# Kernel optimization log

Hardware: AMD Instinct MI355X
Metric: run time of the kernel (lower is better)

The kernel has to match this reference:

```python
import jax, jax.numpy as jnp
import numpy as np

B, C, H, W = 64, 256, 14, 14
K = 9
HID = 256   # EdgeAgg hidden_channels = in_channels
OUT = 512   # out_channels = 2*in_channels (required by final reshape)


def _knn(q, kset, k):
    # ViG dense_knn_matrix: squared-distance knn, top-k of -dist (self-loop may be included)
    qs = jnp.sum(q * q, -1)
    ks = jnp.sum(kset * kset, -1)
    dist = qs[:, :, None] - 2.0 * jnp.einsum('bnc,bmc->bnm', q, kset) + ks[:, None, :]
    _, idx = jax.lax.top_k(-dist, k)   # (B,N,k) neighbor indices into kset
    return idx


def _edgeconv_add(feat, nbr, validf, w, b):
    # PyG EdgeConv(nn=Linear, aggr='add') with per-node valid-edge mask:
    #   out[i] = sum_{j in valid nbrs(i)} cat(x_i, x_j - x_i) @ w + b
    # nn is linear, so aggregate neighbor diffs BEFORE the matmul (same math, less traffic).
    Cf = feat.shape[-1]
    wa, wb = w[:Cf], w[Cf:]
    deg = jnp.sum(validf, -1, keepdims=True)                   # (B,N,1)
    xj = feat[jnp.arange(feat.shape[0])[:, None, None], nbr]   # (B,N,k,C) gather
    sum_xj = jnp.einsum('bnkc,bnk->bnc', xj, validf)
    return deg * (feat @ wa + b) + (sum_xj - deg * feat) @ wb


def _forward(x, fc1_w, fc1_b, fc2_w, fc2_b, fce_w, fce_b, inout_w, inout_b,
             attn_w, attn_b, upd_w, upd_b, kp_w, kp_b, enc_w, enc_b,
             mu_w, mu_b, dec_w, dec_b, T):
    k = dec_w.shape[-1]
    b_, c_, h_, w_ = x.shape
    n = h_ * w_
    xs = x.reshape(b_, c_, n)                       # (B,C,N)
    x_sp = jnp.transpose(xs, (0, 2, 1))             # (B,N,C) true spatial node feats for knn
    x_sp_d = jax.lax.stop_gradient(x_sp)            # original detaches before knn
    x_nbr = _knn(x_sp_d, x_sp_d, k)
    # temporal roll across the T frames of each clip
    y_sp = jnp.roll(x_sp.reshape(b_ // T, T, n, c_), -1, axis=1).reshape(b_, n, c_)
    y_nbr = _knn(x_sp_d, jax.lax.stop_gradient(y_sp), k)
    # faithful to original: x.view(B*N, C) reinterprets the contiguous (B,C,N) buffer
    x_feat = xs.reshape(b_, n, c_)
    y_feat = jnp.transpose(y_sp, (0, 2, 1)).reshape(b_, n, c_)
    # VAE-like K predictor (deterministic z = mu); argmax -> per-node degree in [0,k)
    hk = x_feat.reshape(b_ * n, c_) @ kp_w + kp_b
    hk = jax.nn.relu(hk @ enc_w + enc_b)
    mu = hk @ mu_w + mu_b
    logits = mu @ dec_w + dec_b                     # (B*N, k)
    k_int = jnp.argmax(logits, axis=1)
    # generate_mask: keep the first k_int[i] of node i's k edges
    validf = (jnp.arange(k)[None, :] < k_int[:, None]).astype(x.dtype).reshape(b_, n, k)

    def edge_agg(feat, nbr):
        h1 = jax.nn.relu(_edgeconv_add(feat, nbr, validf, fc1_w, fc1_b))
        h2 = _edgeconv_add(h1, nbr, validf, fc2_w, fc2_b)
        return (h2 @ fce_w + fce_b).reshape(b_ * n, -1)

    x_agg = edge_agg(x_feat, x_nbr)
    y_agg = edge_agg(y_feat, y_nbr)
    scores = (jnp.concatenate([x_agg, y_agg], -1) @ attn_w + attn_b)[:, 0]
    wgt = jax.nn.softmax(scores, axis=0)[:, None]   # softmax over ALL B*N nodes (as in source)
    fused = wgt * x_agg + (1.0 - wgt) * y_agg
    xin = x_feat.reshape(b_ * n, c_) @ inout_w + inout_b
    upd = jax.nn.relu(jnp.concatenate([xin, fused], -1) @ upd_w + upd_b)   # (B*N, 2C)
    return jnp.transpose(upd.reshape(b_, n, 2 * c_), (0, 2, 1)).reshape(b_, 2 * c_, h_, w_)


def setup_inputs():
    key = jax.random.key(0)
    ks = iter(jax.random.split(key, 32))

    def lin(i, o):
        return jax.random.normal(next(ks), (i, o), jnp.float32) / np.sqrt(i)

    def bias(o):
        return jax.random.normal(next(ks), (o,), jnp.float32) * 0.01

    return {
        'x': jax.random.normal(next(ks), (B, C, H, W), jnp.float32),
        'fc1_w': lin(2 * C, HID), 'fc1_b': bias(HID),
        'fc2_w': lin(2 * HID, HID), 'fc2_b': bias(HID),
        'fce_w': lin(HID, OUT), 'fce_b': bias(OUT),
        'inout_w': lin(C, OUT), 'inout_b': bias(OUT),
        'attn_w': lin(2 * OUT, 1), 'attn_b': bias(1),
        'upd_w': lin(2 * OUT, OUT), 'upd_b': bias(OUT),
        'kp_w': lin(C, 500), 'kp_b': bias(500),
        'enc_w': lin(500, 64), 'enc_b': bias(64),
        'mu_w': lin(64, 32), 'mu_b': bias(32),
        'dec_w': lin(32, K), 'dec_b': bias(K),
        'T': 16,
    }


def reference(x, fc1_w, fc1_b, fc2_w, fc2_b, fce_w, fce_b, inout_w, inout_b,
              attn_w, attn_b, upd_w, upd_b, kp_w, kp_b, enc_w, enc_b,
              mu_w, mu_b, dec_w, dec_b, T):
    return _forward(x, fc1_w, fc1_b, fc2_w, fc2_b, fce_w, fce_b, inout_w, inout_b,
                    attn_w, attn_b, upd_w, upd_b, kp_w, kp_b, enc_w, enc_b,
                    mu_w, mu_b, dec_w, dec_b, T)
```

## Files before the change

kernel.cpp:

```cpp
#include <hip/hip_runtime.h>
#include <cstddef>
#include <cstdint>

constexpr int BATCH = 64;
constexpr int CH    = 256;
constexpr int NPT   = 196;
constexpr int ROWS  = BATCH * NPT;
constexpr int BSTRIDE = CH * NPT;
constexpr int KNB   = 8;
constexpr int DSTR  = 208;

typedef __bf16 bf16x8 __attribute__((ext_vector_type(8)));
typedef __bf16 bf16x4 __attribute__((ext_vector_type(4)));
typedef _Float16 f16x8 __attribute__((ext_vector_type(8)));
typedef float  f32x4  __attribute__((ext_vector_type(4)));
typedef unsigned long long u64;

__device__ __forceinline__ int src_batch(int b) {
    return (b & ~15) | ((b + 1) & 15);
}

__device__ __forceinline__ void gload_lds16(const void* g, void* l) {
    __builtin_amdgcn_global_load_lds(
        (const __attribute__((address_space(1))) void*)g,
        (__attribute__((address_space(3))) void*)l, 16, 0, 0);
}

__device__ __forceinline__ int xcd_swz(int lin, int nwg) {
    int q = nwg >> 3;
    return (lin & 7) * q + (lin >> 3);
}

__global__ __launch_bounds__(256) void front_kernel(const float* __restrict__ x,
        _Float16* __restrict__ XH, _Float16* __restrict__ XL,
        __bf16* __restrict__ XB, float* __restrict__ qs,
        const float* __restrict__ fc1_w, const float* __restrict__ fc2_w,
        const float* __restrict__ fce_w, const float* __restrict__ upd_w,
        const float* __restrict__ kp_w, const float* __restrict__ kp_b,
        const float* __restrict__ enc_w, const float* __restrict__ enc_b,
        const float* __restrict__ mu_w, const float* __restrict__ mu_b,
        const float* __restrict__ dec_w, const float* __restrict__ dec_b,
        const float* __restrict__ inout_w, const float* __restrict__ inout_b,
        const float* __restrict__ upd_b,
        __bf16* __restrict__ W1catT, __bf16* __restrict__ W2catT,
        __bf16* __restrict__ fcet, __bf16* __restrict__ updC,
        float* __restrict__ KW1, float* __restrict__ kb1,
        float* __restrict__ KW2, float* __restrict__ kb2,
        float* __restrict__ bcomp, int* __restrict__ smcnt) {
    __shared__ __attribute__((aligned(16))) char smem[16896];
    float (*tile)[65] = (float(*)[65])smem;
    int bid = blockIdx.x;
    int t = threadIdx.x;
    if (bid < 1024) {
        int m0 = (bid & 3) * 64, c0 = ((bid >> 2) & 3) * 64, b = bid >> 4;
        const float* xb = x + (size_t)b * BSTRIDE;
        #pragma unroll
        for (int s = 0; s < 16; ++s) {
            int idx = s * 256 + t;
            int cc = idx >> 6, mm = idx & 63;
            int m = m0 + mm;
            float v = (m < NPT) ? xb[(size_t)(c0 + cc) * NPT + m] : 0.f;
            tile[cc][mm] = v;
            if (m < NPT)
                XB[(size_t)b * BSTRIDE + (size_t)(c0 + cc) * NPT + m] = (__bf16)v;
        }
        __syncthreads();
        #pragma unroll
        for (int s = 0; s < 16; ++s) {
            int idx = s * 256 + t;
            int mm = idx >> 6, cc = idx & 63;
            float v = tile[cc][mm];
            _Float16 h = (_Float16)v;
            size_t off = ((size_t)b * 256 + (m0 + mm)) * 256 + c0 + cc;
            XH[off] = h;
            XL[off] = (_Float16)(v - (float)h);
        }
    } else if (bid < 1088) {
        int b = bid - 1024;
        int m = t;
        if (m >= NPT) return;
        const float* xb = x + (size_t)b * BSTRIDE;
        float acc = 0.f;
        for (int c = 0; c < CH; ++c) {
            float v = xb[c * NPT + m];
            acc = fmaf(v, v, acc);
        }
        qs[b * NPT + m] = acc;
    } else {
        int pbid = bid - 1088;
        if (pbid == 0 && t == 0) smcnt[0] = 0;
        if (pbid < 64) {
            const float* W = (pbid < 32) ? fc1_w : fc2_w;
            __bf16* WT = (pbid < 32) ? W1catT : W2catT;
            int local = pbid & 31;
            int n0 = (local >> 2) * 64, k0 = (local & 3) * 64;
            #pragma unroll
            for (int s = 0; s < 16; ++s) {
                int idx = s * 256 + t;
                int kk = idx >> 6, nn = idx & 63;
                float v;
                if (n0 < 256)
                    v = W[(size_t)(k0 + kk) * 256 + n0 + nn] -
                        W[(size_t)(k0 + kk + 256) * 256 + n0 + nn];
                else
                    v = W[(size_t)(k0 + kk + 256) * 256 + (n0 - 256) + nn];
                tile[kk][nn] = v;
            }
            __syncthreads();
            #pragma unroll
            for (int s = 0; s < 16; ++s) {
                int idx = s * 256 + t;
                int nn = idx >> 6, kk = idx & 63;
                WT[(size_t)(n0 + nn) * 256 + k0 + kk] = (__bf16)tile[kk][nn];
            }
        } else if (pbid < 96) {
            int local = pbid - 64;
            int n0 = (local >> 2) * 64, k0 = (local & 3) * 64;
            #pragma unroll
            for (int s = 0; s < 16; ++s) {
                int idx = s * 256 + t;
                int kk = idx >> 6, nn = idx & 63;
                tile[kk][nn] = fce_w[(size_t)(k0 + kk) * 512 + n0 + nn];
            }
            __syncthreads();
            #pragma unroll
            for (int s = 0; s < 16; ++s) {
                int idx = s * 256 + t;
                int nn = idx >> 6, kk = idx & 63;
                fcet[(size_t)(n0 + nn) * 256 + k0 + kk] = (__bf16)tile[kk][nn];
            }
        } else if (pbid < 160) {
            int local = pbid - 96;
            int k0 = (local >> 3) * 64, n0 = (local & 7) * 64;
            #pragma unroll
            for (int s = 0; s < 16; ++s) {
                int idx = s * 256 + t;
                int kk = idx >> 6, nn = idx & 63;
                tile[kk][nn] = upd_w[(size_t)(512 + k0 + kk) * 512 + n0 + nn];
            }
            __syncthreads();
            #pragma unroll
            for (int s = 0; s < 16; ++s) {
                int idx = s * 256 + t;
                int nn = idx >> 6, kk = idx & 63;
                updC[(size_t)(n0 + nn) * 768 + 256 + k0 + kk] = (__bf16)tile[kk][nn];
            }
        } else if (pbid < 224) {
            int i = (pbid - 160) * 4 + (t >> 6);
            int j = t & 63;
            double acc = 0.0;
            for (int k = 0; k < 500; ++k)
                acc += (double)kp_w[(size_t)i * 500 + k] * (double)enc_w[(size_t)k * 64 + j];
            KW1[i * 64 + j] = (float)acc;
        } else if (pbid == 224) {
            int j = t;
            if (j < 64) {
                double acc = (double)enc_b[j];
                for (int k = 0; k < 500; ++k)
                    acc += (double)kp_b[k] * (double)enc_w[(size_t)k * 64 + j];
                kb1[j] = (float)acc;
            }
        } else if (pbid < 228) {
            int e = (pbid - 225) * 256 + t;
            if (e < 576) {
                int i = e / 9, j = e - (e / 9) * 9;
                double acc = 0.0;
                for (int k = 0; k < 32; ++k)
                    acc += (double)mu_w[(size_t)i * 32 + k] * (double)dec_w[(size_t)k * 9 + j];
                KW2[e] = (float)acc;
            } else if (e < 585) {
                int j = e - 576;
                double acc = (double)dec_b[j];
                for (int k = 0; k < 32; ++k)
                    acc += (double)mu_b[k] * (double)dec_w[(size_t)k * 9 + j];
                kb2[j] = (float)acc;
            }
        } else if (pbid < 740) {
            int e = (pbid - 228) * 256 + t;
            int k = e >> 9, n = e & 511;
            double acc = 0.0;
            for (int j = 0; j < 512; ++j)
                acc += (double)inout_w[(size_t)k * 512 + j] * (double)upd_w[(size_t)j * 512 + n];
            updC[(size_t)n * 768 + k] = (__bf16)(float)acc;
        } else {
            int n = (pbid - 740) * 256 + t;
            double acc = (double)upd_b[n];
            for (int j = 0; j < 512; ++j)
                acc += (double)inout_b[j] * (double)upd_w[(size_t)j * 512 + n];
            bcomp[n] = (float)acc;
        }
    }
}

__global__ __launch_bounds__(256) void gram_kint(const _Float16* __restrict__ XH,
        const _Float16* __restrict__ XL, const float* __restrict__ qs,
        float* __restrict__ Dw, const float* __restrict__ x,
        const float* __restrict__ W1, const float* __restrict__ b1,
        const float* __restrict__ W2, const float* __restrict__ b2,
        int* __restrict__ kint, float* __restrict__ degf) {
    __shared__ __attribute__((aligned(16))) char smem[21056];
    int bid = blockIdx.x;
    int t = threadIdx.x;
    if (bid < 2048) {
        _Float16* Ah = (_Float16*)smem;
        _Float16* Al = Ah + 2048;
        _Float16* Bh = Al + 2048;
        _Float16* Bl = Bh + 2048;
        int nid = xcd_swz(bid, 2048);
        int job = nid >> 4;
        int tile = nid & 15;
        int by = tile >> 2, bx = tile & 3;
        int r0 = by * 64, c0 = bx * 64;
        int qb = (job < 64) ? job : job - 64;
        int kb = (job < 64) ? qb : src_batch(qb);
        int w = t >> 6, l = t & 63;
        int lr = l & 15, lg = l >> 4;
        int wr = (w >> 1) * 32, wc = (w & 1) * 32;
        const _Float16* qh = XH + (size_t)qb * 65536;
        const _Float16* ql = XL + (size_t)qb * 65536;
        const _Float16* kh = XH + (size_t)kb * 65536;
        const _Float16* kl = XL + (size_t)kb * 65536;
        f32x4 acc[2][2] = {};
        for (int k0 = 0; k0 < 256; k0 += 32) {
            {
                int row = w * 16 + (l >> 2);
                int cb = (l & 3) * 8;
                size_t goA = (size_t)(r0 + row) * 256 + k0 + cb;
                size_t goB = (size_t)(c0 + row) * 256 + k0 + cb;
                gload_lds16(qh + goA, Ah + w * 512);
                gload_lds16(ql + goA, Al + w * 512);
                gload_lds16(kh + goB, Bh + w * 512);
                gload_lds16(kl + goB, Bl + w * 512);
            }
            asm volatile("s_waitcnt vmcnt(0)" ::: "memory");
            __syncthreads();
            f16x8 ah[2], alv[2], bh[2], blv[2];
            #pragma unroll
            for (int mi = 0; mi < 2; ++mi) {
                ah[mi]  = *(const f16x8*)(Ah + (wr + mi * 16 + lr) * 32 + lg * 8);
                alv[mi] = *(const f16x8*)(Al + (wr + mi * 16 + lr) * 32 + lg * 8);
            }
            #pragma unroll
            for (int ni = 0; ni < 2; ++ni) {
                bh[ni]  = *(const f16x8*)(Bh + (wc + ni * 16 + lr) * 32 + lg * 8);
                blv[ni] = *(const f16x8*)(Bl + (wc + ni * 16 + lr) * 32 + lg * 8);
            }
            #pragma unroll
            for (int mi = 0; mi < 2; ++mi)
                #pragma unroll
                for (int ni = 0; ni < 2; ++ni) {
                    acc[mi][ni] = __builtin_amdgcn_mfma_f32_16x16x32_f16(
                        ah[mi], bh[ni], acc[mi][ni], 0, 0, 0);
                    acc[mi][ni] = __builtin_amdgcn_mfma_f32_16x16x32_f16(
                        ah[mi], blv[ni], acc[mi][ni], 0, 0, 0);
                    acc[mi][ni] = __builtin_amdgcn_mfma_f32_16x16x32_f16(
                        alv[mi], bh[ni], acc[mi][ni], 0, 0, 0);
                }
            __syncthreads();
        }
        const float* qsq = qs + qb * NPT;
        const float* qsk = qs + kb * NPT;
        float ksv[2];
        #pragma unroll
        for (int ni = 0; ni < 2; ++ni) {
            int col = c0 + wc + ni * 16 + lr;
            ksv[ni] = (col < NPT) ? qsk[col] : 0.f;
        }
        #pragma unroll
        for (int mi = 0; mi < 2; ++mi) {
            #pragma unroll
            for (int r = 0; r < 4; ++r) {
                if (r0 + wr + mi * 16 + r >= NPT) continue;
                int grow = r0 + wr + mi * 16 + lg * 4 + r;
                if (grow >= NPT) continue;
                float qq = qsq[grow];
                size_t rbase = ((size_t)job * NPT + grow) * DSTR;
                #pragma unroll
                for (int ni = 0; ni < 2; ++ni) {
                    int col = c0 + wc + ni * 16 + lr;
                    if (col < NPT)
                        Dw[rbase + col] = qq - 2.f * acc[mi][ni][r] + ksv[ni];
                }
            }
        }
    } else {
        float (*xr)[256] = (float(*)[256])smem;
        float (*ebuf)[64] = (float(*)[64])(smem + 16384);
        float (*lg2)[9]  = (float(*)[9])(smem + 20480);
        int r0 = (bid - 2048) * 16;
        const float4* xg = (const float4*)(x + (size_t)r0 * 256);
        float4* xs = (float4*)&xr[0][0];
        #pragma unroll
        for (int s = 0; s < 4; ++s) xs[s * 256 + t] = xg[s * 256 + t];
        __syncthreads();
        int w = t >> 6, l = t & 63;
        {
            float bb = b1[l];
            float a0 = bb, a1 = bb, a2 = bb, a3 = bb;
            const float* x0 = xr[w * 4 + 0];
            const float* x1 = xr[w * 4 + 1];
            const float* x2 = xr[w * 4 + 2];
            const float* x3 = xr[w * 4 + 3];
            for (int c = 0; c < 256; ++c) {
                float wv = W1[c * 64 + l];
                a0 = fmaf(x0[c], wv, a0);
                a1 = fmaf(x1[c], wv, a1);
                a2 = fmaf(x2[c], wv, a2);
                a3 = fmaf(x3[c], wv, a3);
            }
            ebuf[w * 4 + 0][l] = fmaxf(a0, 0.f);
            ebuf[w * 4 + 1][l] = fmaxf(a1, 0.f);
            ebuf[w * 4 + 2][l] = fmaxf(a2, 0.f);
            ebuf[w * 4 + 3][l] = fmaxf(a3, 0.f);
        }
        __syncthreads();
        int rr = t >> 4, cc = t & 15;
        if (cc < 9) {
            float acc = b2[cc];
            for (int j = 0; j < 64; ++j)
                acc = fmaf(ebuf[rr][j], W2[j * 9 + cc], acc);
            lg2[rr][cc] = acc;
        }
        __syncthreads();
        if (cc == 0) {
            float best = lg2[rr][0];
            int bi = 0;
            #pragma unroll
            for (int j = 1; j < 9; ++j)
                if (lg2[rr][j] > best) { best = lg2[rr][j]; bi = j; }
            kint[r0 + rr] = bi;
            degf[r0 + rr] = (float)bi;
        }
    }
}

__global__ __launch_bounds__(256) void topk_kernel(const float* __restrict__ Dw,
                                                   int* __restrict__ nbr) {
    __shared__ u64 lists[64][4][8];
    int t = threadIdx.x;
    int lrow = t >> 2, q = t & 3;
    int rowid = blockIdx.x * 64 + lrow;
    const float* rp = Dw + (size_t)rowid * DSTR + q * 52;
    u64 kreg[8];
    #pragma unroll
    for (int p = 0; p < 8; ++p) kreg[p] = ~0ull;
    for (int s4 = 0; s4 < 13; ++s4) {
        f32x4 dv = *(const f32x4*)(rp + s4 * 4);
        #pragma unroll
        for (int e = 0; e < 4; ++e) {
            int col = q * 52 + s4 * 4 + e;
            unsigned u = __float_as_uint(dv[e]);
            u = (u & 0x80000000u) ? ~u : (u | 0x80000000u);
            u64 key = (col < NPT) ? (((u64)u << 32) | (unsigned)col) : ~0ull;
            if (key < kreg[7]) {
                #pragma unroll
                for (int p = 0; p < 8; ++p) {
                    u64 mn = (key < kreg[p]) ? key : kreg[p];
                    u64 mx = (key < kreg[p]) ? kreg[p] : key;
                    kreg[p] = mn; key = mx;
                }
            }
        }
    }
    #pragma unroll
    for (int p = 0; p < 8; ++p) lists[lrow][q][p] = kreg[p];
    __syncthreads();
    if (q == 0) {
        const u64* c = &lists[lrow][0][0];
        int p0 = 0, p1 = 0, p2 = 0, p3 = 0;
        #pragma unroll
        for (int it = 0; it < 8; ++it) {
            u64 v0 = c[p0], v1 = c[8 + p1], v2 = c[16 + p2], v3 = c[24 + p3];
            u64 best = v0; int bj = 0;
            if (v1 < best) { best = v1; bj = 1; }
            if (v2 < best) { best = v2; bj = 2; }
            if (v3 < best) { best = v3; bj = 3; }
            if (bj == 0) p0 = (p0 < 7) ? p0 + 1 : 7;
            else if (bj == 1) p1 = (p1 < 7) ? p1 + 1 : 7;
            else if (bj == 2) p2 = (p2 < 7) ? p2 + 1 : 7;
            else p3 = (p3 < 7) ? p3 + 1 : 7;
            nbr[(size_t)rowid * KNB + it] = (int)(best & 0xffffffffu);
        }
    }
}

template<int STAGE, int RELU>
__global__ __launch_bounds__(256) void combine_kernel(const __bf16* __restrict__ P,
        const int* __restrict__ nbr, const int* __restrict__ kint_,
        const float* __restrict__ degf, const float* __restrict__ bias,
        __bf16* __restrict__ H) {
    int g = threadIdx.x >> 6, lane = threadIdx.x & 63;
    int nid = xcd_swz(blockIdx.x, 2 * ROWS / 4);
    int r = nid * 4 + g;
    int branch = (r >= ROWS);
    int rr = r - branch * ROWS;
    int b = rr / NPT, i = rr - b * NPT;
    size_t srow, mbase;
    if constexpr (STAGE == 1) {
        int fb = branch ? src_batch(b) : b;
        srow = (size_t)fb * NPT + i;
        mbase = (size_t)fb * NPT;
    } else {
        srow = (size_t)r;
        mbase = (size_t)branch * ROWS + (size_t)b * NPT;
    }
    const int* nb = nbr + (size_t)branch * ((size_t)ROWS * KNB) + (size_t)rr * KNB;
    bf16x4 sv = *(const bf16x4*)(P + srow * 512 + lane * 4);
    float4 bv = *(const float4*)(bias + lane * 4);
    float s0 = 0.f, s1 = 0.f, s2 = 0.f, s3 = 0.f;
    int kk = kint_[rr];
    for (int tt = 0; tt < kk; ++tt) {
        int m = nb[tt];
        bf16x4 v = *(const bf16x4*)(P + (mbase + m) * 512 + 256 + lane * 4);
        s0 += (float)v[0]; s1 += (float)v[1]; s2 += (float)v[2]; s3 += (float)v[3];
    }
    float dg = degf[rr];
    float o0 = fmaf(dg, (float)sv[0] + bv.x, s0);
    float o1 = fmaf(dg, (float)sv[1] + bv.y, s1);
    float o2 = fmaf(dg, (float)sv[2] + bv.z, s2);
    float o3 = fmaf(dg, (float)sv[3] + bv.w, s3);
    if constexpr (RELU) {
        o0 = fmaxf(o0, 0.f); o1 = fmaxf(o1, 0.f);
        o2 = fmaxf(o2, 0.f); o3 = fmaxf(o3, 0.f);
    }
    bf16x4 ov;
    ov[0] = (__bf16)o0; ov[1] = (__bf16)o1; ov[2] = (__bf16)o2; ov[3] = (__bf16)o3;
    *(bf16x4*)(H + (size_t)r * 256 + lane * 4) = ov;
}

template<int FLAGS, int CONCAT>
__global__ __launch_bounds__(256) void mfma_gemm(
    const __bf16* __restrict__ A0, const __bf16* __restrict__ A1,
    const __bf16* __restrict__ WT, const float* __restrict__ bias,
    float* __restrict__ Cf, __bf16* __restrict__ Cb, int K, int N,
    const float* __restrict__ aw, float* __restrict__ scp,
    const float* __restrict__ wgt) {
    constexpr int SMEMB = (FLAGS & 8) ? (128 * 129 * 4) : (2 * 128 * 64 * 2);
    __shared__ __attribute__((aligned(16))) char smem[SMEMB];
    __bf16* As = (__bf16*)smem;
    __bf16* Bs = As + 128 * 64;
    int lin = blockIdx.x + 4 * blockIdx.y;
    int nid = xcd_swz(lin, 4 * gridDim.y);
    int bx = nid & 3, by = nid >> 2;
    int t = threadIdx.x, w = t >> 6, l = t & 63;
    int r0 = by * 128, c0 = bx * 128;
    int lr = l & 15, lg = l >> 4;
    int wr = (w >> 1) * 64, wc = (w & 1) * 64;
    f32x4 acc[4][4] = {};
    for (int k0 = 0; k0 < K; k0 += 64) {
        #pragma unroll
        for (int i = 0; i < 4; ++i) {
            int row = (w * 4 + i) * 8 + (l >> 3);
            int c8 = l & 7;
            if constexpr (CONCAT == 2) {
                if (k0 < 256) {
                    gload_lds16(A0 + (size_t)(r0 + row) * 256 + k0 + c8 * 8,
                                As + (w * 4 + i) * 512);
                } else {
                    int kk2 = k0 - 256 + c8 * 8;
                    size_t gr = (size_t)(r0 + row);
                    bf16x8 xa = *(const bf16x8*)(A1 + gr * 512 + kk2);
                    bf16x8 ya = *(const bf16x8*)(A1 + ((size_t)ROWS + gr) * 512 + kk2);
                    float wv = wgt[gr];
                    bf16x8 mx;
                    #pragma unroll
                    for (int j = 0; j < 8; ++j)
                        mx[j] = (__bf16)(wv * (float)xa[j] + (1.f - wv) * (float)ya[j]);
                    *(bf16x8*)(As + (w * 4 + i) * 512 + l * 8) = mx;
                }
            } else {
                gload_lds16(A0 + (size_t)(r0 + row) * K + k0 + c8 * 8,
                            As + (w * 4 + i) * 512);
            }
            gload_lds16(WT + (size_t)(c0 + row) * K + k0 + c8 * 8,
                        Bs + (w * 4 + i) * 512);
        }
        asm volatile("s_waitcnt vmcnt(0)" ::: "memory");
        __syncthreads();
        #pragma unroll
        for (int ks = 0; ks < 2; ++ks) {
            bf16x8 af[4], bfr[4];
            #pragma unroll
            for (int mi = 0; mi < 4; ++mi)
                af[mi] = *(const bf16x8*)(As + (wr + mi * 16 + lr) * 64 + ks * 32 + lg * 8);
            #pragma unroll
            for (int ni = 0; ni < 4; ++ni)
                bfr[ni] = *(const bf16x8*)(Bs + (wc + ni * 16 + lr) * 64 + ks * 32 + lg * 8);
            #pragma unroll
            for (int mi = 0; mi < 4; ++mi)
                #pragma unroll
                for (int ni = 0; ni < 4; ++ni)
                    acc[mi][ni] = __builtin_amdgcn_mfma_f32_16x16x32_bf16(
                        af[mi], bfr[ni], acc[mi][ni], 0, 0, 0);
        }
        __syncthreads();
    }
    if constexpr ((FLAGS & 8) != 0) {
        float* tile = (float*)smem;
        #pragma unroll
        for (int mi = 0; mi < 4; ++mi)
            #pragma unroll
            for (int r = 0; r < 4; ++r) {
                int rrow = wr + mi * 16 + lg * 4 + r;
                #pragma unroll
                for (int ni = 0; ni < 4; ++ni) {
                    int ccol = wc + ni * 16 + lr;
                    float v = acc[mi][ni][r];
                    if (bias) v += bias[c0 + ccol];
                    if constexpr ((FLAGS & 1) != 0) v = fmaxf(v, 0.f);
                    tile[rrow * 129 + ccol] = v;
                }
            }
        __syncthreads();
        int cc = t >> 6, rr2 = t & 63;
        #pragma unroll
        for (int cs = 0; cs < 128; cs += 4) {
            #pragma unroll
            for (int h = 0; h < 2; ++h) {
                int row = r0 + rr2 + h * 64;
                int bb = row / NPT, ii = row - bb * NPT;
                Cf[((size_t)bb * 512 + (c0 + cc + cs)) * NPT + ii] =
                    tile[(rr2 + h * 64) * 129 + cc + cs];
            }
        }
    } else if constexpr ((FLAGS & 16) != 0) {
        int half = (r0 >= ROWS) ? 1 : 0;
        float ps[4][4] = {};
        #pragma unroll
        for (int mi = 0; mi < 4; ++mi)
            #pragma unroll
            for (int r = 0; r < 4; ++r) {
                int row = r0 + wr + mi * 16 + lg * 4 + r;
                #pragma unroll
                for (int ni = 0; ni < 4; ++ni) {
                    int col = c0 + wc + ni * 16 + lr;
                    float v = acc[mi][ni][r] + bias[col];
                    Cb[(size_t)row * N + col] = (__bf16)v;
                    ps[mi][r] = fmaf(v, aw[half * 512 + col], ps[mi][r]);
                }
            }
        #pragma unroll
        for (int m = 1; m <= 8; m <<= 1)
            #pragma unroll
            for (int mi = 0; mi < 4; ++mi)
                #pragma unroll
                for (int r = 0; r < 4; ++r)
                    ps[mi][r] += __shfl_xor(ps[mi][r], m, 64);
        if (lr == 0) {
            int slot = half * 8 + bx * 2 + (w & 1);
            #pragma unroll
            for (int mi = 0; mi < 4; ++mi)
                #pragma unroll
                for (int r = 0; r < 4; ++r) {
                    int sr = r0 - half * ROWS + wr + mi * 16 + lg * 4 + r;
                    scp[(size_t)slot * ROWS + sr] = ps[mi][r];
                }
        }
    } else {
        #pragma unroll
        for (int mi = 0; mi < 4; ++mi) {
            #pragma unroll
            for (int r = 0; r < 4; ++r) {
                int row = r0 + wr + mi * 16 + lg * 4 + r;
                #pragma unroll
                for (int ni = 0; ni < 4; ++ni) {
                    int col = c0 + wc + ni * 16 + lr;
                    float v = acc[mi][ni][r];
                    if (bias) v += bias[col];
                    if constexpr ((FLAGS & 1) != 0) v = fmaxf(v, 0.f);
                    if constexpr ((FLAGS & 4) != 0)
                        Cb[(size_t)row * N + col] = (__bf16)v;
                    else
                        Cf[(size_t)row * N + col] = v;
                }
            }
        }
    }
}

__global__ __launch_bounds__(256) void softmax_all(const float* __restrict__ scp,
        const float* __restrict__ ab, float* __restrict__ scores,
        float* __restrict__ mpart, float* __restrict__ spart,
        int* __restrict__ cnt, float* __restrict__ wgt) {
    __shared__ float red[256];
    __shared__ float MS[2];
    __shared__ bool islast;
    int t = threadIdx.x;
    int sr = blockIdx.x * 256 + t;
    float s = ab[0];
    #pragma unroll
    for (int i = 0; i < 16; ++i) s += scp[(size_t)i * ROWS + sr];
    scores[sr] = s;
    red[t] = s; __syncthreads();
    for (int off = 128; off; off >>= 1) {
        if (t < off) red[t] = fmaxf(red[t], red[t + off]);
        __syncthreads();
    }
    float mb = red[0]; __syncthreads();
    red[t] = expf(s - mb); __syncthreads();
    for (int off = 128; off; off >>= 1) {
        if (t < off) red[t] += red[t + off];
        __syncthreads();
    }
    if (t == 0) {
        mpart[blockIdx.x] = mb;
        spart[blockIdx.x] = red[0];
        __threadfence();
        int old = atomicAdd(cnt, 1);
        islast = (old == 48);
    }
    __syncthreads();
    if (!islast) return;
    __threadfence();
    if (t == 0) {
        float M = mpart[0];
        for (int i = 1; i < 49; ++i) M = fmaxf(M, mpart[i]);
        float S = 0.f;
        for (int i = 0; i < 49; ++i) S += spart[i] * expf(mpart[i] - M);
        MS[0] = M; MS[1] = S;
        cnt[0] = 0;
    }
    __syncthreads();
    float M = MS[0], denom = MS[1];
    for (int i = t; i < ROWS; i += 256)
        wgt[i] = expf(scores[i] - M) / denom;
}

extern "C" void kernel_launch(void* const* d_in, const int* in_sizes, int n_in,
                              void* d_out, int out_size, void* d_ws, size_t ws_size,
                              hipStream_t stream) {
    (void)in_sizes; (void)n_in; (void)out_size; (void)ws_size;
    const float* x       = (const float*)d_in[0];
    const float* fc1_w   = (const float*)d_in[1];
    const float* fc1_b   = (const float*)d_in[2];
    const float* fc2_w   = (const float*)d_in[3];
    const float* fc2_b   = (const float*)d_in[4];
    const float* fce_w   = (const float*)d_in[5];
    const float* fce_b   = (const float*)d_in[6];
    const float* inout_w = (const float*)d_in[7];
    const float* inout_b = (const float*)d_in[8];
    const float* attn_w  = (const float*)d_in[9];
    const float* attn_b  = (const float*)d_in[10];
    const float* upd_w   = (const float*)d_in[11];
    const float* upd_b   = (const float*)d_in[12];
    const float* kp_w    = (const float*)d_in[13];
    const float* kp_b    = (const float*)d_in[14];
    const float* enc_w   = (const float*)d_in[15];
    const float* enc_b   = (const float*)d_in[16];
    const float* mu_w    = (const float*)d_in[17];
    const float* mu_b    = (const float*)d_in[18];
    const float* dec_w   = (const float*)d_in[19];
    const float* dec_b   = (const float*)d_in[20];
    float* out = (float*)d_out;

    char* base = (char*)d_ws;
    size_t o = 0;
    auto alloc = [&](size_t bytes) -> void* {
        void* p = base + o;
        o += (bytes + 255) & ~(size_t)255;
        return p;
    };
    float* qs     = (float*)alloc(ROWS * 4);
    float* degf   = (float*)alloc(ROWS * 4);
    float* scores = (float*)alloc(ROWS * 4);
    float* wgt    = (float*)alloc(ROWS * 4);
    int*   kint   = (int*)  alloc(ROWS * 4);
    float* KW1    = (float*)alloc(256 * 64 * 4);
    float* kb1    = (float*)alloc(64 * 4);
    float* KW2    = (float*)alloc(64 * 9 * 4);
    float* kb2    = (float*)alloc(9 * 4);
    float* bcomp  = (float*)alloc(512 * 4);
    float* scp    = (float*)alloc((size_t)16 * ROWS * 4);
    float* mpart  = (float*)alloc(64 * 4);
    float* spart  = (float*)alloc(64 * 4);
    int*   smcnt  = (int*)  alloc(256);
    int*   nbr    = (int*)  alloc((size_t)128 * NPT * KNB * 4);
    char*  regD   = (char*) alloc((size_t)ROWS * 512 * 2);
    __bf16* XB    = (__bf16*)alloc((size_t)ROWS * 256 * 2);
    __bf16* H1    = (__bf16*)alloc((size_t)2 * ROWS * 256 * 2);
    __bf16* H2    = (__bf16*)alloc((size_t)2 * ROWS * 256 * 2);
    char*  regAGG = (char*) alloc((size_t)2 * ROWS * 512 * 4);
    __bf16* W1catT= (__bf16*)alloc((size_t)512 * 256 * 2);
    __bf16* W2catT= (__bf16*)alloc((size_t)512 * 256 * 2);
    __bf16* fcet  = (__bf16*)alloc((size_t)512 * 256 * 2);
    __bf16* updC  = (__bf16*)alloc((size_t)512 * 768 * 2);
    __bf16* P1buf = (__bf16*)regD;
    _Float16* XSPH = (_Float16*)regAGG;
    _Float16* XSPL = XSPH + (size_t)64 * 256 * 256;
    float* Dw     = (float*)(regAGG + (size_t)17 * 1024 * 1024);
    __bf16* P2buf = (__bf16*)regAGG;
    __bf16* AGGb  = (__bf16*)regAGG;
    __bf16* XAGGb = AGGb;

    front_kernel<<<1830, 256, 0, stream>>>(x, XSPH, XSPL, XB, qs,
                                           fc1_w, fc2_w, fce_w, upd_w,
                                           kp_w, kp_b, enc_w, enc_b,
                                           mu_w, mu_b, dec_w, dec_b,
                                           inout_w, inout_b, upd_b,
                                           W1catT, W2catT, fcet, updC,
                                           KW1, kb1, KW2, kb2, bcomp, smcnt);

    gram_kint<<<2832, 256, 0, stream>>>(XSPH, XSPL, qs, Dw, x,
                                        KW1, kb1, KW2, kb2, kint, degf);
    topk_kernel<<<392, 256, 0, stream>>>(Dw, nbr);

    mfma_gemm<4, 0><<<dim3(4, 98), 256, 0, stream>>>(
        XB, nullptr, W1catT, nullptr, nullptr, P1buf, 256, 512,
        nullptr, nullptr, nullptr);
    combine_kernel<1, 1><<<2 * ROWS / 4, 256, 0, stream>>>(
        P1buf, nbr, kint, degf, fc1_b, H1);

    mfma_gemm<4, 0><<<dim3(4, 196), 256, 0, stream>>>(
        H1, nullptr, W2catT, nullptr, nullptr, P2buf, 256, 512,
        nullptr, nullptr, nullptr);
    combine_kernel<2, 0><<<2 * ROWS / 4, 256, 0, stream>>>(
        P2buf, nbr, kint, degf, fc2_b, H2);

    mfma_gemm<20, 0><<<dim3(4, 196), 256, 0, stream>>>(
        H2, nullptr, fcet, fce_b, nullptr, AGGb, 256, 512,
        attn_w, scp, nullptr);

    softmax_all<<<49, 256, 0, stream>>>(scp, attn_b, scores, mpart, spart,
                                        smcnt, wgt);

    mfma_gemm<9, 2><<<dim3(4, 98), 256, 0, stream>>>(
        XB, XAGGb, updC, bcomp, out, nullptr, 768, 512,
        nullptr, nullptr, wgt);
}
```

Measured before the change: 224.7 us.

## Fuse top-k selection with first GEMM launch and register-block weight precompute

Merges the top-k neighbor selection kernel and the first XB×W1catT MFMA GEMM into a single launch, with block index deciding the role, so the two independent workloads share the GPU and one launch is dropped. It also restructures the inout_w×upd_w weight-composition precompute in the front kernel so each thread computes a 2×2 output block, reusing loads and cutting block count from 512 to 128. The fused GEMM is a hand-inlined single-buffered version with no load/compute overlap, and the larger shared memory allocation also applies to the top-k blocks, which can lower their occupancy.

```diff
diff --git a/kernel.cpp b/kernel.cpp
--- a/kernel.cpp
+++ b/kernel.cpp
@@ -175,15 +175,26 @@
                     acc += (double)mu_b[k] * (double)dec_w[(size_t)k * 9 + j];
                 kb2[j] = (float)acc;
             }
-        } else if (pbid < 740) {
-            int e = (pbid - 228) * 256 + t;
-            int k = e >> 9, n = e & 511;
-            double acc = 0.0;
-            for (int j = 0; j < 512; ++j)
-                acc += (double)inout_w[(size_t)k * 512 + j] * (double)upd_w[(size_t)j * 512 + n];
-            updC[(size_t)n * 768 + k] = (__bf16)(float)acc;
+        } else if (pbid < 356) {
+            int k0 = (pbid - 228) * 2;
+            int n = t;
+            double a00 = 0.0, a01 = 0.0, a10 = 0.0, a11 = 0.0;
+            const float* iw0 = inout_w + (size_t)k0 * 512;
+            const float* iw1 = iw0 + 512;
+            for (int j = 0; j < 512; ++j) {
+                double u0 = (double)upd_w[(size_t)j * 512 + n];
+                double u1 = (double)upd_w[(size_t)j * 512 + n + 256];
+                double w0 = (double)iw0[j];
+                double w1 = (double)iw1[j];
+                a00 += w0 * u0; a01 += w0 * u1;
+                a10 += w1 * u0; a11 += w1 * u1;
+            }
+            updC[(size_t)n * 768 + k0]           = (__bf16)(float)a00;
+            updC[(size_t)(n + 256) * 768 + k0]   = (__bf16)(float)a01;
+            updC[(size_t)n * 768 + k0 + 1]       = (__bf16)(float)a10;
+            updC[(size_t)(n + 256) * 768 + k0 + 1] = (__bf16)(float)a11;
         } else {
-            int n = (pbid - 740) * 256 + t;
+            int n = (pbid - 356) * 256 + t;
             double acc = (double)upd_b[n];
             for (int j = 0; j < 512; ++j)
                 acc += (double)inout_b[j] * (double)upd_w[(size_t)j * 512 + n];
@@ -334,52 +345,111 @@
     }
 }
 
-__global__ __launch_bounds__(256) void topk_kernel(const float* __restrict__ Dw,
-                                                   int* __restrict__ nbr) {
-    __shared__ u64 lists[64][4][8];
+__global__ __launch_bounds__(256) void topk_p1(const float* __restrict__ Dw,
+        int* __restrict__ nbr, const __bf16* __restrict__ XB,
+        const __bf16* __restrict__ W1catT, __bf16* __restrict__ P1) {
+    __shared__ __attribute__((aligned(16))) char smem[32768];
+    int bid = blockIdx.x;
     int t = threadIdx.x;
-    int lrow = t >> 2, q = t & 3;
-    int rowid = blockIdx.x * 64 + lrow;
-    const float* rp = Dw + (size_t)rowid * DSTR + q * 52;
-    u64 kreg[8];
-    #pragma unroll
-    for (int p = 0; p < 8; ++p) kreg[p] = ~0ull;
-    for (int s4 = 0; s4 < 13; ++s4) {
-        f32x4 dv = *(const f32x4*)(rp + s4 * 4);
-        #pragma unroll
-        for (int e = 0; e < 4; ++e) {
-            int col = q * 52 + s4 * 4 + e;
-            unsigned u = __float_as_uint(dv[e]);
-            u = (u & 0x80000000u) ? ~u : (u | 0x80000000u);
-            u64 key = (col < NPT) ? (((u64)u << 32) | (unsigned)col) : ~0ull;
-            if (key < kreg[7]) {
-                #pragma unroll
-                for (int p = 0; p < 8; ++p) {
-                    u64 mn = (key < kreg[p]) ? key : kreg[p];
-                    u64 mx = (key < kreg[p]) ? kreg[p] : key;
-                    kreg[p] = mn; key = mx;
-                }
-            }
-        }
-    }
-    #pragma unroll
-    for (int p = 0; p < 8; ++p) lists[lrow][q][p] = kreg[p];
-    __syncthreads();
-    if (q == 0) {
-        const u64* c = &lists[lrow][0][0];
-        int p0 = 0, p1 = 0, p2 = 0, p3 = 0;
-        #pragma unroll
-        for (int it = 0; it < 8; ++it) {
-            u64 v0 = c[p0], v1 = c[8 + p1], v2 = c[16 + p2], v3 = c[24 + p3];
-            u64 best = v0; int bj = 0;
-            if (v1 < best) { best = v1; bj = 1; }
-            if (v2 < best) { best = v2; bj = 2; }
-            if (v3 < best) { best = v3; bj = 3; }
-            if (bj == 0) p0 = (p0 < 7) ? p0 + 1 : 7;
-            else if (bj == 1) p1 = (p1 < 7) ? p1 + 1 : 7;
-            else if (bj == 2) p2 = (p2 < 7) ? p2 + 1 : 7;
-            else p3 = (p3 < 7) ? p3 + 1 : 7;
-            nbr[(size_t)rowid * KNB + it] = (int)(best & 0xffffffffu);
+    if (bid < 392) {
+        u64 (*lists)[4][8] = (u64(*)[4][8])smem;
+        int lrow = t >> 2, q = t & 3;
+        int rowid = bid * 64 + lrow;
+        const float* rp = Dw + (size_t)rowid * DSTR + q * 52;
+        u64 kreg[8];
+        #pragma unroll
+        for (int p = 0; p < 8; ++p) kreg[p] = ~0ull;
+        for (int s4 = 0; s4 < 13; ++s4) {
+            f32x4 dv = *(const f32x4*)(rp + s4 * 4);
+            #pragma unroll
+            for (int e = 0; e < 4; ++e) {
+                int col = q * 52 + s4 * 4 + e;
+                unsigned u = __float_as_uint(dv[e]);
+                u = (u & 0x80000000u) ? ~u : (u | 0x80000000u);
+                u64 key = (col < NPT) ? (((u64)u << 32) | (unsigned)col) : ~0ull;
+                if (key < kreg[7]) {
+                    #pragma unroll
+                    for (int p = 0; p < 8; ++p) {
+                        u64 mn = (key < kreg[p]) ? key : kreg[p];
+                        u64 mx = (key < kreg[p]) ? kreg[p] : key;
+                        kreg[p] = mn; key = mx;
+                    }
+                }
+            }
+        }
+        #pragma unroll
+        for (int p = 0; p < 8; ++p) lists[lrow][q][p] = kreg[p];
+        __syncthreads();
+        if (q == 0) {
+            const u64* c = &lists[lrow][0][0];
+            int p0 = 0, p1 = 0, p2 = 0, p3 = 0;
+            #pragma unroll
+            for (int it = 0; it < 8; ++it) {
+                u64 v0 = c[p0], v1 = c[8 + p1], v2 = c[16 + p2], v3 = c[24 + p3];
+                u64 best = v0; int bj = 0;
+                if (v1 < best) { best = v1; bj = 1; }
+                if (v2 < best) { best = v2; bj = 2; }
+                if (v3 < best) { best = v3; bj = 3; }
+                if (bj == 0) p0 = (p0 < 7) ? p0 + 1 : 7;
+                else if (bj == 1) p1 = (p1 < 7) ? p1 + 1 : 7;
+                else if (bj == 2) p2 = (p2 < 7) ? p2 + 1 : 7;
+                else p3 = (p3 < 7) ? p3 + 1 : 7;
+                nbr[(size_t)rowid * KNB + it] = (int)(best & 0xffffffffu);
+            }
+        }
+    } else {
+        __bf16* As = (__bf16*)smem;
+        __bf16* Bs = As + 128 * 64;
+        int lin = bid - 392;
+        int nid = xcd_swz(lin, 392);
+        int bx = nid & 3, by = nid >> 2;
+        int w = t >> 6, l = t & 63;
+        int r0 = by * 128, c0 = bx * 128;
+        int lr = l & 15, lg = l >> 4;
+        int wr = (w >> 1) * 64, wc = (w & 1) * 64;
+        constexpr int K = 256, N = 512;
+        f32x4 acc[4][4] = {};
+        for (int k0 = 0; k0 < K; k0 += 64) {
+            #pragma unroll
+            for (int i = 0; i < 4; ++i) {
+                int row = (w * 4 + i) * 8 + (l >> 3);
+                int c8 = l & 7;
+                gload_lds16(XB + (size_t)(r0 + row) * K + k0 + c8 * 8,
+                            As + (w * 4 + i) * 512);
+                gload_lds16(W1catT + (size_t)(c0 + row) * K + k0 + c8 * 8,
+                            Bs + (w * 4 + i) * 512);
+            }
+            asm volatile("s_waitcnt vmcnt(0)" ::: "memory");
+            __syncthreads();
+            #pragma unroll
+            for (int ks = 0; ks < 2; ++ks) {
+                bf16x8 af[4], bfr[4];
+                #pragma unroll
+                for (int mi = 0; mi < 4; ++mi)
+                    af[mi] = *(const bf16x8*)(As + (wr + mi * 16 + lr) * 64 + ks * 32 + lg * 8);
+                #pragma unroll
+                for (int ni = 0; ni < 4; ++ni)
+                    bfr[ni] = *(const bf16x8*)(Bs + (wc + ni * 16 + lr) * 64 + ks * 32 + lg * 8);
+                #pragma unroll
+                for (int mi = 0; mi < 4; ++mi)
+                    #pragma unroll
+                    for (int ni = 0; ni < 4; ++ni)
+                        acc[mi][ni] = __builtin_amdgcn_mfma_f32_16x16x32_bf16(
+                            af[mi], bfr[ni], acc[mi][ni], 0, 0, 0);
+            }
+            __syncthreads();
+        }
+        #pragma unroll
+        for (int mi = 0; mi < 4; ++mi) {
+            #pragma unroll
+            for (int r = 0; r < 4; ++r) {
+                int row = r0 + wr + mi * 16 + lg * 4 + r;
+                #pragma unroll
+                for (int ni = 0; ni < 4; ++ni) {
+                    int col = c0 + wc + ni * 16 + lr;
+                    P1[(size_t)row * N + col] = (__bf16)acc[mi][ni][r];
+                }
+            }
         }
     }
 }
@@ -692,7 +762,7 @@
     __bf16* AGGb  = (__bf16*)regAGG;
     __bf16* XAGGb = AGGb;
 
-    front_kernel<<<1830, 256, 0, stream>>>(x, XSPH, XSPL, XB, qs,
+    front_kernel<<<1446, 256, 0, stream>>>(x, XSPH, XSPL, XB, qs,
                                            fc1_w, fc2_w, fce_w, upd_w,
                                            kp_w, kp_b, enc_w, enc_b,
                                            mu_w, mu_b, dec_w, dec_b,
@@ -702,11 +772,9 @@
 
     gram_kint<<<2832, 256, 0, stream>>>(XSPH, XSPL, qs, Dw, x,
                                         KW1, kb1, KW2, kb2, kint, degf);
-    topk_kernel<<<392, 256, 0, stream>>>(Dw, nbr);
-
-    mfma_gemm<4, 0><<<dim3(4, 98), 256, 0, stream>>>(
-        XB, nullptr, W1catT, nullptr, nullptr, P1buf, 256, 512,
-        nullptr, nullptr, nullptr);
+
+    topk_p1<<<784, 256, 0, stream>>>(Dw, nbr, XB, W1catT, P1buf);
+
     combine_kernel<1, 1><<<2 * ROWS / 4, 256, 0, stream>>>(
         P1buf, nbr, kint, degf, fc1_b, H1);
 
```

New measurement: 230.8 us. 2.7% more time.
